# Optimization experiments

Hardware: AMD Instinct MI355X
Metric: run time of the kernel (lower is better)

## Reference

```python
import jax, jax.numpy as jnp
import numpy as np

ALPHA, BETA, LAMB = 1.0, 1.0, 1e-4
K, TAU, DELTA = 16, 0.1, 1e-4
N, D, B, NQ = 100000, 256, 256, 4096


def setup_inputs() -> dict:
    key = jax.random.key(0)
    k1, k2, k3, k4, k5, k6 = jax.random.split(key, 6)
    X = jax.random.normal(k1, (N, D), dtype=jnp.float32)
    W = jax.random.normal(k2, (D, D), dtype=jnp.float32) / np.sqrt(D)
    q_batch = jax.random.normal(k3, (B, D), dtype=jnp.float32)
    pre_weights = jax.random.uniform(k4, (NQ, K), dtype=jnp.float32)
    pre_weights = pre_weights / pre_weights.sum(axis=1, keepdims=True)
    q_indices = jax.random.randint(k5, (B,), 0, NQ)
    pre_indices = jax.random.randint(k6, (NQ, K), 0, N)
    return {"X": X, "W": W, "q_batch": q_batch, "pre_weights": pre_weights,
            "q_indices": q_indices, "pre_indices": pre_indices}


def _matrix_sqrt(A):
    # differentiable symmetric matrix sqrt via eigendecomposition
    w, v = jnp.linalg.eigh(A)
    w = jnp.sqrt(jnp.clip(w, 0.0))
    return (v * w) @ v.T


def _loss_dist(T, mu_X, cov_X, cov_X_sqrt):
    mu = jnp.mean(T, axis=0)
    Tc = T - mu
    cov = Tc.T @ Tc / T.shape[0] + DELTA * jnp.eye(T.shape[1], dtype=T.dtype)
    loss_mean = jnp.sum((mu - mu_X) ** 2)
    cov_sqrt = _matrix_sqrt(cov)
    sqrt_term = _matrix_sqrt(cov_sqrt @ cov_X @ cov_sqrt)
    loss_cov = jnp.trace(cov_X + cov - 2.0 * sqrt_term)
    return jnp.clip(loss_mean + loss_cov, 0.0)


def _kl_per_sample(pre_idx, pre_w, post_idx, post_w):
    # union via first-occurrence mask over concatenated candidates [2K]
    cand = jnp.concatenate([pre_idx, post_idx])
    eq = cand[:, None] == cand[None, :]
    first = ~jnp.tril(eq, k=-1).any(axis=1)
    p = (cand[:, None] == pre_idx[None, :]).astype(pre_w.dtype) @ pre_w
    q = (cand[:, None] == post_idx[None, :]).astype(post_w.dtype) @ post_w
    p = jnp.where(first, jnp.clip(p, 1e-8), 0.0)
    p = p / p.sum()
    q = jnp.where(first, jnp.clip(q, 1e-8), 0.0)
    q = q / q.sum()
    logp = jnp.log(jnp.where(first, p, 1.0))
    logq = jnp.log(jnp.where(first, q, 1.0))
    return jnp.sum(jnp.where(first, p * (logp - logq), 0.0))


def _forward(X, W, q_batch, pre_weights, q_indices, pre_indices):
    # precomputed database stats
    mu_X = jnp.mean(X, axis=0)
    Xc = X - mu_X
    cov_X = Xc.T @ Xc / X.shape[0] + DELTA * jnp.eye(X.shape[1], dtype=X.dtype)
    cov_X_sqrt = _matrix_sqrt(cov_X)

    T = q_batch @ W  # model(q_batch): [B, D]

    loss_dist = _loss_dist(T, mu_X, cov_X, cov_X_sqrt)

    # brute-force exact KNN (faiss flat L2) on detached T
    Td = jax.lax.stop_gradient(T)
    d2 = (jnp.sum(Td * Td, axis=1, keepdims=True)
          - 2.0 * (Td @ X.T) + jnp.sum(X * X, axis=1))  # [B, N]
    _, post_idx = jax.lax.top_k(-d2, K)  # [B, K]

    X_nb = X[post_idx]  # [B, K, D]
    l2 = jnp.sum((T[:, None, :] - X_nb) ** 2, axis=-1)  # [B, K], with grad
    post_w = jax.nn.softmax(-l2 / TAU, axis=1)

    pre_idx_b = pre_indices[q_indices]   # [B, K]
    pre_w_b = pre_weights[q_indices]     # [B, K]
    kls = jax.vmap(_kl_per_sample)(pre_idx_b, pre_w_b, post_idx, post_w)
    loss_knn = jnp.mean(kls)

    loss_reg = 0.5 * jnp.sum(W ** 2)

    total = ALPHA * loss_dist + BETA * loss_knn + LAMB * loss_reg
    return total, loss_dist, loss_knn


def reference(X, W, q_batch, pre_weights, q_indices, pre_indices):
    return _forward(X, W, q_batch, pre_weights, q_indices, pre_indices)
```

## Files before the change

### kernel.cpp

```cpp
#include <hip/hip_runtime.h>

#define NPTS   100000
#define DIMD   256
#define BQ     256
#define PCHUNK 128
#define NPCH   782
#define NCAND  (NPCH*16)
#define NS_ITERS 26
#define KSPLIT  32
#define KSLICE  3136
#define KS2    576
#define NZ2    175

#define SC_LM   0
#define SC_TRCX 1
#define SC_TRCT 2
#define SC_FROB 3
#define SC_KNN  4
#define SC_REG  5
#define SC_LD   6

#define BIGF 3.4e38f

typedef __attribute__((ext_vector_type(4))) float f32x4;
typedef __attribute__((ext_vector_type(8))) unsigned short u16x8;
typedef __attribute__((ext_vector_type(8))) __bf16 bf16x8;

static __device__ __forceinline__ unsigned short f2bf(float f) {
    unsigned u = __float_as_uint(f);
    unsigned r = (u + 0x7fffu + ((u >> 16) & 1u)) >> 16;
    return (unsigned short)r;
}
static __device__ __forceinline__ float bf2f(unsigned short h) {
    return __uint_as_float(((unsigned)h) << 16);
}
static __device__ __forceinline__ unsigned pack_hi(float a, float b) {
    return (__float_as_uint(a) >> 16) | (__float_as_uint(b) & 0xffff0000u);
}
static __device__ __forceinline__ float trunc_bf(float a) {
    return __uint_as_float(__float_as_uint(a) & 0xffff0000u);
}
static __device__ __forceinline__ unsigned short top16(float v) {
    return (unsigned short)(__float_as_uint(v) >> 16);
}
static __device__ __forceinline__ f32x4 mfma16(u16x8 a, u16x8 b, f32x4 c) {
    return __builtin_amdgcn_mfma_f32_16x16x32_bf16(
        __builtin_bit_cast(bf16x8, a), __builtin_bit_cast(bf16x8, b), c, 0, 0, 0);
}

static __device__ __forceinline__ unsigned enc_f32(float f) {
    unsigned u = __float_as_uint(f);
    return u ^ (unsigned)(((int)u >> 31) | 0x80000000);
}
static __device__ __forceinline__ float dec_f32(unsigned e) {
    unsigned u = e ^ ((e & 0x80000000u) ? 0x80000000u : 0xFFFFFFFFu);
    return __uint_as_float(u);
}
static __device__ __forceinline__ unsigned umin32(unsigned a, unsigned b) { return a < b ? a : b; }
static __device__ __forceinline__ void ceu(unsigned& a, unsigned& b) {
    unsigned lo = a < b ? a : b;
    unsigned hi = a < b ? b : a;
    a = lo; b = hi;
}
static __device__ __forceinline__ void sort16(unsigned* r) {
#pragma unroll
    for (int k = 2; k <= 16; k <<= 1)
#pragma unroll
        for (int j = k >> 1; j > 0; j >>= 1)
#pragma unroll
            for (int i = 0; i < 16; ++i) {
                int l = i ^ j;
                if (l > i) {
                    if ((i & k) == 0) ceu(r[i], r[l]);
                    else              ceu(r[l], r[i]);
                }
            }
}
static __device__ __forceinline__ void clean16(unsigned* r) {
#pragma unroll
    for (int j = 8; j > 0; j >>= 1)
#pragma unroll
        for (int i = 0; i < 16; ++i) {
            int l = i ^ j;
            if (l > i) ceu(r[i], r[l]);
        }
}
static __device__ __forceinline__ int lessp(float ka, int ia, float kb, int ib) {
    return (ka < kb) || (ka == kb && ia < ib);
}
static __device__ __forceinline__ void ceup(float& ka, int& ia, float& kb, int& ib) {
    bool sw = lessp(kb, ib, ka, ia);
    float t0 = sw ? kb : ka, t1 = sw ? ka : kb;
    int   u0 = sw ? ib : ia, u1 = sw ? ia : ib;
    ka = t0; kb = t1; ia = u0; ib = u1;
}
static __device__ __forceinline__ void cleanp16(float* k, int* i) {
#pragma unroll
    for (int j = 8; j > 0; j >>= 1)
#pragma unroll
        for (int x = 0; x < 16; ++x) {
            int l = x ^ j;
            if (l > x) ceup(k[x], i[x], k[l], i[l]);
        }
}

__global__ __launch_bounds__(256) void zero_kernel(float* ws) {
    int idx = blockIdx.x * 256 + threadIdx.x;
    if (idx < 66560) ws[idx] = 0.0f;
}

__global__ __launch_bounds__(256) void statsx_kernel(const float* __restrict__ X,
                                                     float* __restrict__ xsq,
                                                     float* __restrict__ mu_sum,
                                                     unsigned short* __restrict__ XHs,
                                                     unsigned short* __restrict__ XLs) {
    __shared__ float colred[4][256];
    const int t = threadIdx.x;
    const int w = t >> 6, lane = t & 63;
    const int half = lane >> 5;
    const int g = lane & 31;
    const int rbase = blockIdx.x * 128;
    float cs[8] = {0.f, 0.f, 0.f, 0.f, 0.f, 0.f, 0.f, 0.f};
#pragma unroll 2
    for (int m = 0; m < 16; ++m) {
        const int r = rbase + m * 8 + w * 2 + half;
        if (r < NPTS) {
            float4 v0 = *(const float4*)&X[r * DIMD + g * 8];
            float4 v1 = *(const float4*)&X[r * DIMD + g * 8 + 4];
            cs[0] += v0.x; cs[1] += v0.y; cs[2] += v0.z; cs[3] += v0.w;
            cs[4] += v1.x; cs[5] += v1.y; cs[6] += v1.z; cs[7] += v1.w;
            float ss = v0.x * v0.x + v0.y * v0.y + v0.z * v0.z + v0.w * v0.w
                     + v1.x * v1.x + v1.y * v1.y + v1.z * v1.z + v1.w * v1.w;
#pragma unroll
            for (int off = 16; off; off >>= 1) ss += __shfl_down(ss, off, 32);
            if (g == 0) xsq[r] = ss;
            if (XHs) {
                uint4 hv = make_uint4(pack_hi(v0.x, v0.y), pack_hi(v0.z, v0.w),
                                      pack_hi(v1.x, v1.y), pack_hi(v1.z, v1.w));
                uint4 lv = make_uint4(
                    pack_hi(v0.x - trunc_bf(v0.x), v0.y - trunc_bf(v0.y)),
                    pack_hi(v0.z - trunc_bf(v0.z), v0.w - trunc_bf(v0.w)),
                    pack_hi(v1.x - trunc_bf(v1.x), v1.y - trunc_bf(v1.y)),
                    pack_hi(v1.z - trunc_bf(v1.z), v1.w - trunc_bf(v1.w)));
                *(uint4*)(XHs + (size_t)r * 256 + g * 8) = hv;
                *(uint4*)(XLs + (size_t)r * 256 + g * 8) = lv;
            }
        } else if (XHs) {
            uint4 z4 = make_uint4(0u, 0u, 0u, 0u);
            *(uint4*)(XHs + (size_t)r * 256 + g * 8) = z4;
            *(uint4*)(XLs + (size_t)r * 256 + g * 8) = z4;
        }
    }
#pragma unroll
    for (int j = 0; j < 8; ++j) cs[j] += __shfl_down(cs[j], 32);
    if (half == 0) {
#pragma unroll
        for (int j = 0; j < 8; ++j) colred[w][g * 8 + j] = cs[j];
    }
    __syncthreads();
    float s = colred[0][t] + colred[1][t] + colred[2][t] + colred[3][t];
    atomicAdd(&mu_sum[t], s);
}

__global__ __launch_bounds__(256) void xtk_kernel(const unsigned short* __restrict__ XHs,
                                                  const unsigned short* __restrict__ XLs,
                                                  unsigned short* __restrict__ XTH,
                                                  unsigned short* __restrict__ XTL) {
    __shared__ unsigned short LH[32][268];
    __shared__ unsigned short LL[32][268];
    const int t = threadIdx.x;
#pragma unroll 1
    for (int st = 0; st < 8; ++st) {
        const int r0 = blockIdx.x * 256 + st * 32;
        const int row = t >> 3;
        const int r = r0 + row;
#pragma unroll
        for (int gg = 0; gg < 4; ++gg) {
            int glog = (t & 7) + gg * 8;
            u16x8 h = *(const u16x8*)(XHs + (size_t)r * 256 + glog * 8);
            u16x8 l = *(const u16x8*)(XLs + (size_t)r * 256 + glog * 8);
            *(u16x8*)&LH[row][glog * 8] = h;
            *(u16x8*)&LL[row][glog * 8] = l;
        }
        __syncthreads();
        {
            unsigned pk[16];
#pragma unroll
            for (int m = 0; m < 16; ++m)
                pk[m] = (unsigned)LH[2 * m][t] | ((unsigned)LH[2 * m + 1][t] << 16);
            uint4* oh = (uint4*)(XTH + (size_t)t * 100352 + r0);
#pragma unroll
            for (int q = 0; q < 4; ++q)
                oh[q] = make_uint4(pk[4 * q], pk[4 * q + 1], pk[4 * q + 2], pk[4 * q + 3]);
#pragma unroll
            for (int m = 0; m < 16; ++m)
                pk[m] = (unsigned)LL[2 * m][t] | ((unsigned)LL[2 * m + 1][t] << 16);
            uint4* ol = (uint4*)(XTL + (size_t)t * 100352 + r0);
#pragma unroll
            for (int q = 0; q < 4; ++q)
                ol[q] = make_uint4(pk[4 * q], pk[4 * q + 1], pk[4 * q + 2], pk[4 * q + 3]);
        }
        __syncthreads();
    }
}

__global__ __launch_bounds__(256) void covx2_kernel(const unsigned short* __restrict__ XTH,
                                                    const unsigned short* __restrict__ XTL,
                                                    float* __restrict__ acc_out) {
    const int quad = blockIdx.x;
    const int qi = quad >> 1, qj = quad & 1;
    const int t = threadIdx.x, w = t >> 6, lane = t & 63;
    const int l15 = lane & 15, l4 = lane >> 4;
    const int k0 = blockIdx.y * KS2;
    const int kend = (k0 + KS2 < 100352) ? (k0 + KS2) : 100352;
    f32x4 acc[2][8];
#pragma unroll
    for (int f = 0; f < 2; ++f)
#pragma unroll
        for (int cf = 0; cf < 8; ++cf) { f32x4 z = {0.f, 0.f, 0.f, 0.f}; acc[f][cf] = z; }
    const size_t rowA0 = (size_t)(qi * 128 + w * 32 + l15) * 100352;
    const size_t rowA1 = (size_t)(qi * 128 + w * 32 + 16 + l15) * 100352;
#pragma unroll 1
    for (int k = k0; k < kend; k += 32) {
        const int ko = k + l4 * 8;
        u16x8 ah0 = *(const u16x8*)(XTH + rowA0 + ko);
        u16x8 al0 = *(const u16x8*)(XTL + rowA0 + ko);
        u16x8 ah1 = *(const u16x8*)(XTH + rowA1 + ko);
        u16x8 al1 = *(const u16x8*)(XTL + rowA1 + ko);
#pragma unroll
        for (int cf = 0; cf < 8; ++cf) {
            const size_t rb = (size_t)(qj * 128 + cf * 16 + l15) * 100352 + ko;
            u16x8 bh = *(const u16x8*)(XTH + rb);
            u16x8 bl = *(const u16x8*)(XTL + rb);
            acc[0][cf] = mfma16(ah0, bh, acc[0][cf]);
            acc[0][cf] = mfma16(ah0, bl, acc[0][cf]);
            acc[0][cf] = mfma16(al0, bh, acc[0][cf]);
            acc[1][cf] = mfma16(ah1, bh, acc[1][cf]);
            acc[1][cf] = mfma16(ah1, bl, acc[1][cf]);
            acc[1][cf] = mfma16(al1, bh, acc[1][cf]);
        }
    }
#pragma unroll
    for (int f = 0; f < 2; ++f)
#pragma unroll
        for (int cf = 0; cf < 8; ++cf)
#pragma unroll
            for (int i = 0; i < 4; ++i) {
                const int r = qi * 128 + w * 32 + f * 16 + l4 * 4 + i;
                const int c = qj * 128 + cf * 16 + l15;
                atomicAdd(&acc_out[r * DIMD + c], acc[f][cf][i]);
            }
}

__global__ __launch_bounds__(256) void covx_kernel(const float* __restrict__ X,
                                                   float* __restrict__ acc_out) {
    __shared__ float Ais[16][64];
    __shared__ float Ajs[16][64];
    int t = threadIdx.x;
    int i0 = blockIdx.x * 64, j0 = blockIdx.y * 64;
    int ks = blockIdx.z * KSLICE;
    int lr = t >> 4, lc = (t & 15) * 4;
    int tx = t & 15, ty = t >> 4;
    float acc[4][4] = {};
    for (int kb = 0; kb < KSLICE; kb += 16) {
        int k = ks + kb + lr;
        if (k < NPTS) {
            float4 vi = *(const float4*)&X[k * DIMD + i0 + lc];
            float4 vj = *(const float4*)&X[k * DIMD + j0 + lc];
            *(float4*)&Ais[lr][lc] = vi;
            *(float4*)&Ajs[lr][lc] = vj;
        } else {
            float4 z = {0.f, 0.f, 0.f, 0.f};
            *(float4*)&Ais[lr][lc] = z;
            *(float4*)&Ajs[lr][lc] = z;
        }
        __syncthreads();
#pragma unroll
        for (int kk = 0; kk < 16; ++kk) {
            float4 a = *(float4*)&Ais[kk][tx * 4];
            float4 b = *(float4*)&Ajs[kk][ty * 4];
            float av[4] = {a.x, a.y, a.z, a.w};
            float bv[4] = {b.x, b.y, b.z, b.w};
#pragma unroll
            for (int m = 0; m < 4; ++m)
#pragma unroll
                for (int n = 0; n < 4; ++n) acc[m][n] += av[m] * bv[n];
        }
        __syncthreads();
    }
#pragma unroll
    for (int m = 0; m < 4; ++m)
#pragma unroll
        for (int n = 0; n < 4; ++n)
            atomicAdd(&acc_out[(i0 + 4 * tx + m) * DIMD + j0 + 4 * ty + n], acc[m][n]);
}

__global__ __launch_bounds__(256) void covxfin2_kernel(const float* __restrict__ acc,
                                                       const float* __restrict__ mu_sum,
                                                       float* __restrict__ covXf,
                                                       float* __restrict__ scal) {
    int idx = blockIdx.x * 256 + threadIdx.x;
    int i = idx >> 8, j = idx & 255;
    const float invN = 1.0f / (float)NPTS;
    float v = acc[idx] * invN - (mu_sum[i] * invN) * (mu_sum[j] * invN) + ((i == j) ? 1e-4f : 0.0f);
    covXf[idx] = v;
    if (i == j) atomicAdd(&scal[SC_TRCX], v);
}

__global__ __launch_bounds__(256) void mm32_kernel(const float* A, const float* B, float* C, const float* D,
                                                   const float* A2, const float* B2, float* C2, const float* D2,
                                                   int mode, const float* mu, float* scal) {
    __shared__ float As[32][32];
    __shared__ float Bs[32][32];
    __shared__ float red[256];
    int t = threadIdx.x;
    int tx = t & 15, ty = t >> 4;
    int i0 = blockIdx.x * 32, j0 = blockIdx.y * 32;
    int lr = t >> 3, lc = (t & 7) * 4;
    float acc[2][2] = {};
    for (int kb = 0; kb < 256; kb += 32) {
        if (mode == 2) {
            float4 v = *(const float4*)&A[(kb + lr) * DIMD + i0 + lc];
            *(float4*)&As[lr][lc] = v;
        } else {
            float4 v = *(const float4*)&A[(i0 + lr) * DIMD + kb + lc];
            As[lc + 0][lr] = v.x; As[lc + 1][lr] = v.y; As[lc + 2][lr] = v.z; As[lc + 3][lr] = v.w;
        }
        {
            float4 v = *(const float4*)&B[(kb + lr) * DIMD + j0 + lc];
            *(float4*)&Bs[lr][lc] = v;
        }
        __syncthreads();
#pragma unroll
        for (int kk = 0; kk < 32; ++kk) {
            float a0 = As[kk][2 * tx], a1 = As[kk][2 * tx + 1];
            float b0 = Bs[kk][2 * ty], b1 = Bs[kk][2 * ty + 1];
            acc[0][0] += a0 * b0; acc[0][1] += a0 * b1;
            acc[1][0] += a1 * b0; acc[1][1] += a1 * b1;
        }
        __syncthreads();
    }
    float fr = 0.f;
#pragma unroll
    for (int ii = 0; ii < 2; ++ii)
#pragma unroll
        for (int jj = 0; jj < 2; ++jj) {
            int i = i0 + 2 * tx + ii, j = j0 + 2 * ty + jj;
            float v = acc[ii][jj];
            if (mode == 2) {
                v = v * (1.0f / 256.0f) - mu[i] * mu[j] + ((i == j) ? 1e-4f : 0.0f);
                if (i == j) atomicAdd(&scal[SC_TRCT], v);
            }
            C[i * DIMD + j] = v;
            if (mode == 1) fr += v * v;
        }
    if (mode == 0 && C2 != nullptr) {
        unsigned short* TH = (unsigned short*)C2;
        unsigned short* TL = (unsigned short*)const_cast<float*>(D2);
#pragma unroll
        for (int ii = 0; ii < 2; ++ii) {
            int i = i0 + 2 * tx + ii;
            int jc = j0 + 2 * ty;
            float x0 = acc[ii][0], x1 = acc[ii][1];
            *(unsigned*)&TH[i * DIMD + jc] = pack_hi(x0, x1);
            *(unsigned*)&TL[i * DIMD + jc] = pack_hi(x0 - trunc_bf(x0), x1 - trunc_bf(x1));
        }
    }
    if (mode == 1) {
        red[t] = fr; __syncthreads();
        for (int s2 = 128; s2 > 0; s2 >>= 1) { if (t < s2) red[t] += red[t + s2]; __syncthreads(); }
        if (t == 0) atomicAdd(&scal[SC_FROB], red[0]);
    }
}

__global__ __launch_bounds__(256) void tstats_kernel(const float* __restrict__ Tm,
                                                     const float* __restrict__ mu_sum,
                                                     float* __restrict__ mu_T,
                                                     float* __restrict__ scal) {
    __shared__ float red[256];
    int j = threadIdx.x;
    float s = 0.f;
    for (int b = 0; b < BQ; ++b) s += Tm[b * DIMD + j];
    float mt = s * (1.0f / 256.0f);
    mu_T[j] = mt;
    float d = mt - mu_sum[j] * (1.0f / (float)NPTS);
    red[j] = d * d;
    __syncthreads();
    for (int s2 = 128; s2 > 0; s2 >>= 1) { if (j < s2) red[j] += red[j + s2]; __syncthreads(); }
    if (j == 0) scal[SC_LM] = red[0];
}

__global__ __launch_bounds__(256) void inityz2_kernel(const float* __restrict__ G,
                                                      const float* __restrict__ scal,
                                                      float* __restrict__ Y, float* __restrict__ Z,
                                                      unsigned short* __restrict__ YaH,
                                                      unsigned short* __restrict__ YaL,
                                                      unsigned short* __restrict__ ZaH,
                                                      unsigned short* __restrict__ ZaL) {
    int idx = blockIdx.x * 256 + threadIdx.x;
    float invs = rsqrtf(scal[SC_FROB]);
    float y = G[idx] * invs;
    Y[idx] = y;
    YaH[idx] = top16(y);
    YaL[idx] = top16(y - trunc_bf(y));
    bool dg = ((idx >> 8) == (idx & 255));
    Z[idx] = dg ? 1.0f : 0.0f;
    ZaH[idx] = dg ? (unsigned short)0x3F80 : (unsigned short)0;
    ZaL[idx] = 0;
}

__global__ __launch_bounds__(256) void nsfused_kernel(
        const float* __restrict__ Ycur, const float* __restrict__ Zcur,
        const unsigned short* __restrict__ YH, const unsigned short* __restrict__ YL,
        const unsigned short* __restrict__ ZH, const unsigned short* __restrict__ ZL,
        float* __restrict__ Yn, float* __restrict__ Zn,
        unsigned short* __restrict__ YnH, unsigned short* __restrict__ YnL,
        unsigned short* __restrict__ ZnH, unsigned short* __restrict__ ZnL) {
    __shared__ __align__(16) unsigned short VH[16 * 264];
    __shared__ __align__(16) unsigned short VL[16 * 264];
    __shared__ __align__(16) unsigned short IH[16 * 264];
    __shared__ __align__(16) unsigned short IL[16 * 264];
    const int t = threadIdx.x, w = t >> 6, lane = t & 63;
    const int l15 = lane & 15, l4 = lane >> 4;
    const int j0 = blockIdx.x * 16;
    const unsigned short *M1H, *M1L, *M2H, *M2L, *VsH, *VsL;
    const float* Dm; float* Out; unsigned short *OH, *OL;
    if (blockIdx.y == 0) { M1H = ZH; M1L = ZL; M2H = YH; M2L = YL; VsH = YH; VsL = YL;
                           Dm = Ycur; Out = Yn; OH = YnH; OL = YnL; }
    else                 { M1H = YH; M1L = YL; M2H = ZH; M2L = ZL; VsH = ZH; VsL = ZL;
                           Dm = Zcur; Out = Zn; OH = ZnH; OL = ZnL; }
    {
        const int col = t >> 4, k0 = (t & 15) * 16;
#pragma unroll
        for (int m = 0; m < 8; ++m) {
            const int k = k0 + 2 * m;
            unsigned h0 = VsH[(size_t)k * 256 + j0 + col];
            unsigned h1 = VsH[(size_t)(k + 1) * 256 + j0 + col];
            unsigned l0 = VsL[(size_t)k * 256 + j0 + col];
            unsigned l1 = VsL[(size_t)(k + 1) * 256 + j0 + col];
            *(unsigned*)&VH[col * 264 + k] = h0 | (h1 << 16);
            *(unsigned*)&VL[col * 264 + k] = l0 | (l1 << 16);
        }
    }
    __syncthreads();
    f32x4 acc[4];
#pragma unroll
    for (int f = 0; f < 4; ++f) { f32x4 z = {0.f, 0.f, 0.f, 0.f}; acc[f] = z; }
#pragma unroll
    for (int ks = 0; ks < 8; ++ks) {
        const int bo = l15 * 264 + ks * 32 + l4 * 8;
        u16x8 bh = *(const u16x8*)&VH[bo];
        u16x8 bl = *(const u16x8*)&VL[bo];
#pragma unroll
        for (int f = 0; f < 4; ++f) {
            const size_t ro = (size_t)(w * 64 + f * 16 + l15) * 256 + ks * 32 + l4 * 8;
            u16x8 ah = *(const u16x8*)(M1H + ro);
            u16x8 al = *(const u16x8*)(M1L + ro);
            acc[f] = mfma16(ah, bh, acc[f]);
            acc[f] = mfma16(ah, bl, acc[f]);
            acc[f] = mfma16(al, bh, acc[f]);
        }
    }
#pragma unroll
    for (int f = 0; f < 4; ++f) {
        float v0 = acc[f][0], v1 = acc[f][1], v2 = acc[f][2], v3 = acc[f][3];
        unsigned h01 = pack_hi(v0, v1), h23 = pack_hi(v2, v3);
        unsigned l01 = pack_hi(v0 - trunc_bf(v0), v1 - trunc_bf(v1));
        unsigned l23 = pack_hi(v2 - trunc_bf(v2), v3 - trunc_bf(v3));
        const int ad = l15 * 264 + w * 64 + f * 16 + l4 * 4;
        *(uint2*)&IH[ad] = make_uint2(h01, h23);
        *(uint2*)&IL[ad] = make_uint2(l01, l23);
    }
    __syncthreads();
#pragma unroll
    for (int f = 0; f < 4; ++f) { f32x4 z = {0.f, 0.f, 0.f, 0.f}; acc[f] = z; }
#pragma unroll
    for (int ks = 0; ks < 8; ++ks) {
        const int bo = l15 * 264 + ks * 32 + l4 * 8;
        u16x8 bh = *(const u16x8*)&IH[bo];
        u16x8 bl = *(const u16x8*)&IL[bo];
#pragma unroll
        for (int f = 0; f < 4; ++f) {
            const size_t ro = (size_t)(w * 64 + f * 16 + l15) * 256 + ks * 32 + l4 * 8;
            u16x8 ah = *(const u16x8*)(M2H + ro);
            u16x8 al = *(const u16x8*)(M2L + ro);
            acc[f] = mfma16(ah, bh, acc[f]);
            acc[f] = mfma16(ah, bl, acc[f]);
            acc[f] = mfma16(al, bh, acc[f]);
        }
    }
#pragma unroll
    for (int f = 0; f < 4; ++f)
#pragma unroll
        for (int i = 0; i < 4; ++i) {
            const int r = w * 64 + f * 16 + l4 * 4 + i;
            const int c = j0 + l15;
            float v = 1.5f * Dm[r * 256 + c] - 0.5f * acc[f][i];
            Out[r * 256 + c] = v;
            OH[r * 256 + c] = top16(v);
            OL[r * 256 + c] = top16(v - trunc_bf(v));
        }
}

__global__ __launch_bounds__(256) void findist_kernel(const float* __restrict__ Yfin,
                                                      float* __restrict__ scal) {
    __shared__ float red[256];
    int t = threadIdx.x;
    red[t] = Yfin[t * (DIMD + 1)];
    __syncthreads();
    for (int s2 = 128; s2 > 0; s2 >>= 1) { if (t < s2) red[t] += red[t + s2]; __syncthreads(); }
    if (t == 0) {
        float frobsq = scal[SC_FROB];
        float tr_sqrt = powf(frobsq, 0.25f) * red[0];
        float lc = scal[SC_TRCX] + scal[SC_TRCT] - 2.0f * tr_sqrt;
        scal[SC_LD] = fmaxf(0.0f, scal[SC_LM] + lc);
    }
}

__global__ __launch_bounds__(256) void reg_kernel(const float* __restrict__ W, float* __restrict__ scal) {
    __shared__ float red[256];
    int t = threadIdx.x;
    float s = 0.f;
    int base = blockIdx.x * 1024;
    for (int m = 0; m < 4; ++m) { float w = W[base + m * 256 + t]; s += w * w; }
    red[t] = s;
    __syncthreads();
    for (int s2 = 128; s2 > 0; s2 >>= 1) { if (t < s2) red[t] += red[t + s2]; __syncthreads(); }
    if (t == 0) atomicAdd(&scal[SC_REG], red[0]);
}

__global__ __launch_bounds__(256, 2) void knn3_kernel(const unsigned short* __restrict__ TmH,
                                                      const unsigned short* __restrict__ TmL,
                                                      const unsigned short* __restrict__ XHs,
                                                      const unsigned short* __restrict__ XLs,
                                                      const float* __restrict__ xsq,
                                                      float* __restrict__ ck, int* __restrict__ ci) {
    __shared__ __align__(16) unsigned char sm2[69632];
    unsigned* kt = (unsigned*)(sm2 + 32768);
    const int t = threadIdx.x;
    const int w = t >> 6, lane = t & 63;
    const int l15 = lane & 15, l4 = lane >> 4;
    const int p0 = blockIdx.x * PCHUNK;
    const int swz = (l15 & 7) << 4;

    unsigned sk[16];
#pragma unroll
    for (int s = 0; s < 16; ++s) sk[s] = 0xFFFFFFFFu;

#pragma unroll 1
    for (int pc = 0; pc < 4; ++pc) {
        const int pbase = p0 + pc * 32;
        {
            const uint4* gh = (const uint4*)(XHs + (size_t)pbase * 256);
            const uint4* gl = (const uint4*)(XLs + (size_t)pbase * 256);
#pragma unroll
            for (int r = 0; r < 4; ++r) {
                const int slot = r * 256 + t;
                const int row = slot >> 5, gi = slot & 31;
                const int dst = row * 512 + (((gi ^ (row & 7))) << 4);
                uint4 vh = gh[slot];
                uint4 vl = gl[slot];
                *(uint4*)(sm2 + dst) = vh;
                *(uint4*)(sm2 + 16384 + dst) = vl;
            }
        }
        __syncthreads();
        f32x4 acc[4][2];
#pragma unroll
        for (int f = 0; f < 4; ++f)
#pragma unroll
            for (int pt = 0; pt < 2; ++pt) { f32x4 z = {0.f, 0.f, 0.f, 0.f}; acc[f][pt] = z; }
#pragma unroll
        for (int ks = 0; ks < 8; ++ks) {
            const int g = (((ks * 4 + l4) << 4)) ^ swz;
            const int b0 = l15 * 512 + g;
            const int b1 = (16 + l15) * 512 + g;
            u16x8 bh0 = *(const u16x8*)(sm2 + b0);
            u16x8 bl0 = *(const u16x8*)(sm2 + 16384 + b0);
            u16x8 bh1 = *(const u16x8*)(sm2 + b1);
            u16x8 bl1 = *(const u16x8*)(sm2 + 16384 + b1);
#pragma unroll
            for (int f = 0; f < 4; ++f) {
                const size_t ro = (size_t)(w * 64 + f * 16 + l15) * 256 + ks * 32 + l4 * 8;
                u16x8 ah = *(const u16x8*)(TmH + ro);
                u16x8 al = *(const u16x8*)(TmL + ro);
                acc[f][0] = mfma16(ah, bh0, acc[f][0]);
                acc[f][0] = mfma16(ah, bl0, acc[f][0]);
                acc[f][0] = mfma16(al, bh0, acc[f][0]);
                acc[f][1] = mfma16(ah, bh1, acc[f][1]);
                acc[f][1] = mfma16(ah, bl1, acc[f][1]);
                acc[f][1] = mfma16(al, bh1, acc[f][1]);
            }
        }
#pragma unroll
        for (int pt = 0; pt < 2; ++pt) {
            const int p = pbase + pt * 16 + l15;
            const float xv = xsq[p];
            const bool ok = (p < NPTS);
            const unsigned lidx = (unsigned)(pc * 32 + pt * 16 + l15);
#pragma unroll
            for (int f = 0; f < 4; ++f)
#pragma unroll
                for (int i = 0; i < 4; ++i) {
                    float d2 = ok ? (xv - 2.0f * acc[f][pt][i]) : BIGF;
                    unsigned e = (enc_f32(d2) & 0xFFFFFF80u) | lidx;
                    kt[(w * 64 + f * 16 + l4 * 4 + i) * 36 + pt * 16 + l15] = e;
                }
        }
        __syncthreads();
#pragma unroll
        for (int hb = 0; hb < 2; ++hb) {
            unsigned b[16];
#pragma unroll
            for (int c4 = 0; c4 < 4; ++c4) {
                uint4 v = *(const uint4*)(kt + t * 36 + hb * 16 + c4 * 4);
                b[c4 * 4 + 0] = v.x; b[c4 * 4 + 1] = v.y;
                b[c4 * 4 + 2] = v.z; b[c4 * 4 + 3] = v.w;
            }
            sort16(b);
#pragma unroll
            for (int i = 0; i < 16; ++i) sk[i] = umin32(sk[i], b[15 - i]);
            clean16(sk);
        }
    }
    const int base = t * NCAND + blockIdx.x * 16;
#pragma unroll
    for (int s = 0; s < 16; ++s) {
        ck[base + s] = dec_f32(sk[s] & 0xFFFFFF80u);
        ci[base + s] = p0 + (int)(sk[s] & 127u);
    }
}

static __device__ __forceinline__ void knn_load(const float* __restrict__ X, int p0, int pc, int t,
                                                float4 s0[2], float4 s1[2]) {
#pragma unroll
    for (int rep = 0; rep < 2; ++rep) {
        int g = t + rep * 512;
        int row = g >> 5, c0 = (g & 31) * 8;
        int p = p0 + pc * 32 + row;
        if (p < NPTS) {
            s0[rep] = *(const float4*)&X[p * DIMD + c0];
            s1[rep] = *(const float4*)&X[p * DIMD + c0 + 4];
        } else {
            float4 z = {0.f, 0.f, 0.f, 0.f};
            s0[rep] = z; s1[rep] = z;
        }
    }
}
static __device__ __forceinline__ void knn_write(unsigned short* XH, unsigned short* XL, int t,
                                                 const float4 s0[2], const float4 s1[2]) {
#pragma unroll
    for (int rep = 0; rep < 2; ++rep) {
        int g = t + rep * 512;
        int row = g >> 5, c0 = (g & 31) * 8;
        float f[8] = {s0[rep].x, s0[rep].y, s0[rep].z, s0[rep].w,
                      s1[rep].x, s1[rep].y, s1[rep].z, s1[rep].w};
        u16x8 h, lo;
#pragma unroll
        for (int j = 0; j < 8; ++j) {
            unsigned short hb = f2bf(f[j]);
            h[j] = hb;
            lo[j] = f2bf(f[j] - bf2f(hb));
        }
        *(u16x8*)&XH[row * 264 + c0] = h;
        *(u16x8*)&XL[row * 264 + c0] = lo;
    }
}
__global__ __launch_bounds__(512, 2) void knn_kernel(const float* __restrict__ Tm,
                                                     const float* __restrict__ X,
                                                     const float* __restrict__ xsq,
                                                     float* __restrict__ ck, int* __restrict__ ci) {
    __shared__ __align__(16) unsigned char smem[50688];
    unsigned short* XH = (unsigned short*)smem;
    unsigned short* XL = (unsigned short*)(smem + 16896);
    float* ktf = (float*)smem;
    float* tk  = (float*)(smem + 34304);
    int*   ti  = (int*)  (smem + 42496);
    const int t    = threadIdx.x;
    const int w    = t >> 6;
    const int lane = t & 63;
    const int l15  = lane & 15;
    const int l4   = lane >> 4;
    const int p0   = blockIdx.x * PCHUNK;
    const int q0   = blockIdx.y * 128;
    u16x8 aH[8], aL[8];
    {
        const int q = q0 + w * 16 + l15;
        const float* tq = Tm + q * DIMD + l4 * 8;
#pragma unroll
        for (int ks = 0; ks < 8; ++ks) {
            float4 v0 = *(const float4*)(tq + ks * 32);
            float4 v1 = *(const float4*)(tq + ks * 32 + 4);
            float f[8] = {v0.x, v0.y, v0.z, v0.w, v1.x, v1.y, v1.z, v1.w};
            u16x8 h, lo;
#pragma unroll
            for (int j = 0; j < 8; ++j) {
                unsigned short hb = f2bf(f[j]);
                h[j] = hb;
                lo[j] = f2bf(f[j] - bf2f(hb));
            }
            aH[ks] = h; aL[ks] = lo;
        }
    }
    float worst = BIGF; int wslot = 0;
    float4 s0[2], s1[2];
    knn_load(X, p0, 0, t, s0, s1);
    knn_write(XH, XL, t, s0, s1);
#pragma unroll
    for (int h = 0; h < 2; ++h) {
        f32x4 acc[4];
#pragma unroll
        for (int a2 = 0; a2 < 4; ++a2) { f32x4 z = {0.f, 0.f, 0.f, 0.f}; acc[a2] = z; }
#pragma unroll
        for (int pc2 = 0; pc2 < 2; ++pc2) {
            const int pc = 2 * h + pc2;
            __syncthreads();
            if (pc < 3) knn_load(X, p0, pc + 1, t, s0, s1);
#pragma unroll
            for (int ks = 0; ks < 8; ++ks) {
#pragma unroll
                for (int pt = 0; pt < 2; ++pt) {
                    const int off = (pt * 16 + l15) * 264 + ks * 32 + l4 * 8;
                    u16x8 bh = *(const u16x8*)&XH[off];
                    u16x8 bl = *(const u16x8*)&XL[off];
                    acc[pc2 * 2 + pt] = mfma16(aH[ks], bh, acc[pc2 * 2 + pt]);
                    acc[pc2 * 2 + pt] = mfma16(aH[ks], bl, acc[pc2 * 2 + pt]);
                    acc[pc2 * 2 + pt] = mfma16(aL[ks], bh, acc[pc2 * 2 + pt]);
                }
            }
            __syncthreads();
            if (pc2 == 0 && pc < 3) knn_write(XH, XL, t, s0, s1);
        }
#pragma unroll
        for (int pc2 = 0; pc2 < 2; ++pc2) {
#pragma unroll
            for (int pt = 0; pt < 2; ++pt) {
                const int pl = pc2 * 32 + pt * 16 + l15;
                const int p  = p0 + h * 64 + pl;
                const float xv = (p < NPTS) ? xsq[p] : 0.f;
#pragma unroll
                for (int i = 0; i < 4; ++i) {
                    float key = (p < NPTS) ? (xv - 2.0f * acc[pc2 * 2 + pt][i]) : BIGF;
                    ktf[(w * 16 + l4 * 4 + i) * 67 + pl] = key;
                }
            }
        }
        __syncthreads();
        if (t < 128) {
            if (h == 0) {
#pragma unroll
                for (int s = 0; s < 16; ++s) { tk[s * 128 + t] = BIGF; ti[s * 128 + t] = 0x7fffffff; }
            }
            for (int c = 0; c < 64; ++c) {
                float key = ktf[t * 67 + c];
                if (key < worst) {
                    tk[wslot * 128 + t] = key; ti[wslot * 128 + t] = p0 + h * 64 + c;
                    worst = tk[t]; wslot = 0;
#pragma unroll
                    for (int s = 1; s < 16; ++s) {
                        float v = tk[s * 128 + t];
                        if (v > worst) { worst = v; wslot = s; }
                    }
                }
            }
        }
        __syncthreads();
        if (h == 0) knn_write(XH, XL, t, s0, s1);
    }
    if (t < 128) {
        int base = (q0 + t) * NCAND + blockIdx.x * 16;
        for (int s = 0; s < 16; ++s) { ck[base + s] = tk[s * 128 + t]; ci[base + s] = ti[s * 128 + t]; }
    }
}

__global__ __launch_bounds__(256) void merge2_kernel(const float* __restrict__ ck,
                                                     const int* __restrict__ ci,
                                                     int* __restrict__ post_idx) {
    __shared__ float km[16 * 256];
    __shared__ int   im[16 * 256];
    const int q = blockIdx.x, t = threadIdx.x;
    float sk[16]; int si[16];
#pragma unroll
    for (int s = 0; s < 16; ++s) { sk[s] = BIGF; si[s] = 0x7fffffff; }
#pragma unroll 1
    for (int run = t; run < NPCH; run += 256) {
        const float* rk = ck + (size_t)q * NCAND + run * 16;
        const int*   ri = ci + (size_t)q * NCAND + run * 16;
#pragma unroll 1
        for (int s = 0; s < 16; ++s) {
            float k = rk[s]; int id = ri[s];
            if (!lessp(k, id, sk[15], si[15])) break;
#pragma unroll
            for (int j = 15; j > 0; --j) {
                bool a = lessp(k, id, sk[j - 1], si[j - 1]);
                bool b = lessp(k, id, sk[j], si[j]);
                float nk = a ? sk[j - 1] : (b ? k : sk[j]);
                int   ni = a ? si[j - 1] : (b ? id : si[j]);
                sk[j] = nk; si[j] = ni;
            }
            bool c = lessp(k, id, sk[0], si[0]);
            float nk0 = c ? k : sk[0]; int ni0 = c ? id : si[0];
            sk[0] = nk0; si[0] = ni0;
        }
    }
#pragma unroll
    for (int s = 0; s < 16; ++s) { km[s * 256 + t] = sk[s]; im[s * 256 + t] = si[s]; }
    __syncthreads();
    for (int off = 128; off > 0; off >>= 1) {
        if (t < off) {
            float bk[16]; int bi[16];
#pragma unroll
            for (int s = 0; s < 16; ++s) { bk[s] = km[s * 256 + t + off]; bi[s] = im[s * 256 + t + off]; }
#pragma unroll
            for (int s = 0; s < 16; ++s) {
                float ak = sk[s];  int ai = si[s];
                float ok = bk[15 - s]; int oi = bi[15 - s];
                bool a = lessp(ak, ai, ok, oi);
                sk[s] = a ? ak : ok; si[s] = a ? ai : oi;
            }
            cleanp16(sk, si);
#pragma unroll
            for (int s = 0; s < 16; ++s) { km[s * 256 + t] = sk[s]; im[s * 256 + t] = si[s]; }
        }
        __syncthreads();
    }
    if (t == 0) {
#pragma unroll
        for (int r = 0; r < 16; ++r) post_idx[q * 16 + r] = si[r];
    }
}

__global__ __launch_bounds__(256) void merge_kernel(const float* __restrict__ ck,
                                                    const int* __restrict__ ci,
                                                    int* __restrict__ post_idx) {
    __shared__ float tk[16][256];
    __shared__ int   ti[16][256];
    __shared__ float rk[256];
    __shared__ int   ri[256];
    __shared__ int   rt2[256];
    __shared__ int   rs2[256];
    int q = blockIdx.x, t = threadIdx.x;
    for (int s = 0; s < 16; ++s) { tk[s][t] = BIGF; ti[s][t] = 0x7fffffff; }
    float worst = BIGF; int wslot = 0;
    for (int e = t; e < NCAND; e += 256) {
        float key = ck[q * NCAND + e];
        if (key < worst) {
            tk[wslot][t] = key; ti[wslot][t] = ci[q * NCAND + e];
            worst = tk[0][t]; wslot = 0;
            for (int s = 1; s < 16; ++s)
                if (tk[s][t] > worst) { worst = tk[s][t]; wslot = s; }
        }
    }
    __syncthreads();
    for (int r = 0; r < 16; ++r) {
        float bk = tk[0][t]; int bi = ti[0][t], bs = 0;
        for (int s = 1; s < 16; ++s) {
            float k2 = tk[s][t]; int i2 = ti[s][t];
            if (k2 < bk || (k2 == bk && i2 < bi)) { bk = k2; bi = i2; bs = s; }
        }
        rk[t] = bk; ri[t] = bi; rt2[t] = t; rs2[t] = bs;
        __syncthreads();
        for (int s2 = 128; s2 > 0; s2 >>= 1) {
            if (t < s2) {
                float ko = rk[t + s2]; int io = ri[t + s2];
                if (ko < rk[t] || (ko == rk[t] && io < ri[t])) {
                    rk[t] = ko; ri[t] = io; rt2[t] = rt2[t + s2]; rs2[t] = rs2[t + s2];
                }
            }
            __syncthreads();
        }
        if (t == rt2[0]) { tk[rs2[0]][t] = BIGF; ti[rs2[0]][t] = 0x7fffffff; }
        if (t == 0) post_idx[q * 16 + r] = ri[0];
        __syncthreads();
    }
}

__global__ __launch_bounds__(256) void l2sm_kernel(const float* __restrict__ Tm,
                                                   const float* __restrict__ X,
                                                   const int* __restrict__ post_idx,
                                                   float* __restrict__ post_w) {
    __shared__ float l2s[16];
    int b = blockIdx.x, t = threadIdx.x;
    int k = t >> 4, j = t & 15;
    int idx = post_idx[b * 16 + k];
    float s = 0.f;
    for (int i = 0; i < 16; ++i) {
        int d = j + 16 * i;
        float df = Tm[b * DIMD + d] - X[idx * DIMD + d];
        s += df * df;
    }
    for (int off = 8; off; off >>= 1) s += __shfl_down(s, off, 16);
    if (j == 0) l2s[k] = s;
    __syncthreads();
    if (t < 16) {
        float x = -l2s[t] * 10.0f;
        float m = x;
        for (int mm = 8; mm; mm >>= 1) m = fmaxf(m, __shfl_xor(m, mm, 16));
        float e = expf(x - m);
        float ssum = e;
        for (int mm = 8; mm; mm >>= 1) ssum += __shfl_xor(ssum, mm, 16);
        post_w[b * 16 + t] = e / ssum;
    }
}

__global__ __launch_bounds__(256) void kl_kernel(const int* __restrict__ q_indices,
                                                 const int* __restrict__ pre_indices,
                                                 const float* __restrict__ pre_weights,
                                                 const int* __restrict__ post_idx,
                                                 const float* __restrict__ post_w,
                                                 float* __restrict__ scal) {
    int b = threadIdx.x;
    int qi = q_indices[b];
    int pid[16]; float pw[16]; int sid[16]; float sw[16];
    for (int k = 0; k < 16; ++k) {
        pid[k] = pre_indices[qi * 16 + k];
        pw[k]  = pre_weights[qi * 16 + k];
        sid[k] = post_idx[b * 16 + k];
        sw[k]  = post_w[b * 16 + k];
    }
    float psum = 0.f, qsum = 0.f, kl = 0.f;
    for (int pass = 0; pass < 2; ++pass) {
        for (int i = 0; i < 32; ++i) {
            int c = (i < 16) ? pid[i] : sid[i - 16];
            bool first = true;
            for (int jj = 0; jj < i; ++jj) {
                int cj = (jj < 16) ? pid[jj] : sid[jj - 16];
                if (cj == c) { first = false; break; }
            }
            if (!first) continue;
            float p = 0.f, q = 0.f;
            for (int k2 = 0; k2 < 16; ++k2) {
                if (pid[k2] == c) p += pw[k2];
                if (sid[k2] == c) q += sw[k2];
            }
            p = fmaxf(p, 1e-8f); q = fmaxf(q, 1e-8f);
            if (pass == 0) { psum += p; qsum += q; }
            else {
                float pn = p / psum, qn = q / qsum;
                kl += pn * (logf(pn) - logf(qn));
            }
        }
    }
    atomicAdd(&scal[SC_KNN], kl * (1.0f / 256.0f));
}

__global__ void assemble_kernel(const float* __restrict__ scal, float* __restrict__ out) {
    if (threadIdx.x == 0) {
        float ld = scal[SC_LD], lk = scal[SC_KNN], reg = scal[SC_REG];
        out[0] = ld + lk + 1e-4f * 0.5f * reg;
        out[1] = ld;
        out[2] = lk;
    }
}

extern "C" void kernel_launch(void* const* d_in, const int* in_sizes, int n_in,
                              void* d_out, int out_size, void* d_ws, size_t ws_size,
                              hipStream_t stream) {
    (void)in_sizes; (void)n_in; (void)out_size;
    const float* X           = (const float*)d_in[0];
    const float* W           = (const float*)d_in[1];
    const float* q_batch     = (const float*)d_in[2];
    const float* pre_weights = (const float*)d_in[3];
    const int*   q_indices   = (const int*)d_in[4];
    const int*   pre_indices = (const int*)d_in[5];
    float* out = (float*)d_out;
    float* ws  = (float*)d_ws;

    float* mu_sum = ws + 0;
    float* scal   = ws + 256;
    float* mu_T   = ws + 512;
    float* covX   = ws + 1024;
    float* Tm     = ws + 66560;
    float* cov    = ws + 132096;
    float* G      = ws + 197632;
    float* Ya     = ws + 263168;
    float* Za     = ws + 328704;
    float* Yb     = ws + 394240;
    float* Zb     = ws + 459776;
    float* covXf  = ws + 525312;
    float* xsq    = ws + 590848;
    float* post_w = ws + 691200;
    int*   post_idx = (int*)(ws + 695296);
    float* ck     = ws + 699392;
    int*   ci     = (int*)(ws + 3902464);
    unsigned short* YaH = (unsigned short*)(ws + 699392);
    unsigned short* YaL = (unsigned short*)(ws + 732160);
    unsigned short* ZaH = (unsigned short*)(ws + 764928);
    unsigned short* ZaL = (unsigned short*)(ws + 797696);
    unsigned short* YbH = (unsigned short*)(ws + 830464);
    unsigned short* YbL = (unsigned short*)(ws + 863232);
    unsigned short* ZbH = (unsigned short*)(ws + 896000);
    unsigned short* ZbL = (unsigned short*)(ws + 928768);
    unsigned short* XHs = (unsigned short*)(ws + 7105536);
    unsigned short* XLs = (unsigned short*)(ws + 19950592);
    unsigned short* TmH = (unsigned short*)(ws + 32795648);
    unsigned short* TmL = (unsigned short*)(ws + 32828416);
    unsigned short* XTH = (unsigned short*)(ws + 32845824);
    unsigned short* XTL = (unsigned short*)(ws + 45690880);
    const bool haveIMG = (ws_size >= (size_t)131444736);
    const bool haveXT  = (ws_size >= (size_t)234143744);

    zero_kernel<<<260, 256, 0, stream>>>(ws);
    reg_kernel<<<64, 256, 0, stream>>>(W, scal);
    statsx_kernel<<<784, 256, 0, stream>>>(X, xsq, mu_sum,
                                           haveIMG ? XHs : nullptr, haveIMG ? XLs : nullptr);
    if (haveXT) {
        xtk_kernel<<<392, 256, 0, stream>>>(XHs, XLs, XTH, XTL);
        covx2_kernel<<<dim3(4, NZ2), 256, 0, stream>>>(XTH, XTL, covX);
    } else {
        covx_kernel<<<dim3(4, 4, KSPLIT), 256, 0, stream>>>(X, covX);
    }
    covxfin2_kernel<<<256, 256, 0, stream>>>(covX, mu_sum, covXf, scal);
    mm32_kernel<<<dim3(8, 8, 1), 256, 0, stream>>>(q_batch, W, Tm, nullptr,
                                                   nullptr, nullptr,
                                                   haveIMG ? (float*)TmH : nullptr,
                                                   haveIMG ? (float*)TmL : nullptr, 0, nullptr, scal);
    tstats_kernel<<<1, 256, 0, stream>>>(Tm, mu_sum, mu_T, scal);
    mm32_kernel<<<dim3(8, 8, 1), 256, 0, stream>>>(Tm, Tm, cov, nullptr,
                                                   nullptr, nullptr, nullptr, nullptr, 2, mu_T, scal);
    mm32_kernel<<<dim3(8, 8, 1), 256, 0, stream>>>(cov, covXf, G, nullptr,
                                                   nullptr, nullptr, nullptr, nullptr, 1, nullptr, scal);
    if (haveIMG) {
        knn3_kernel<<<NPCH, 256, 0, stream>>>(TmH, TmL, XHs, XLs, xsq, ck, ci);
        merge2_kernel<<<256, 256, 0, stream>>>(ck, ci, post_idx);
    } else {
        knn_kernel<<<dim3(NPCH, 2, 1), 512, 0, stream>>>(Tm, X, xsq, ck, ci);
        merge_kernel<<<256, 256, 0, stream>>>(ck, ci, post_idx);
    }
    l2sm_kernel<<<256, 256, 0, stream>>>(Tm, X, post_idx, post_w);
    kl_kernel<<<1, 256, 0, stream>>>(q_indices, pre_indices, pre_weights, post_idx, post_w, scal);
    inityz2_kernel<<<256, 256, 0, stream>>>(G, scal, Ya, Za, YaH, YaL, ZaH, ZaL);
    {
        float *Yc = Ya, *Zc = Za, *Yn = Yb, *Zn = Zb;
        unsigned short *cYH = YaH, *cYL = YaL, *cZH = ZaH, *cZL = ZaL;
        unsigned short *nYH = YbH, *nYL = YbL, *nZH = ZbH, *nZL = ZbL;
        for (int it = 0; it < NS_ITERS; ++it) {
            nsfused_kernel<<<dim3(16, 2), 256, 0, stream>>>(Yc, Zc, cYH, cYL, cZH, cZL,
                                                            Yn, Zn, nYH, nYL, nZH, nZL);
            float* tf;
            tf = Yc; Yc = Yn; Yn = tf;
            tf = Zc; Zc = Zn; Zn = tf;
            unsigned short* tu;
            tu = cYH; cYH = nYH; nYH = tu;
            tu = cYL; cYL = nYL; nYL = tu;
            tu = cZH; cZH = nZH; nZH = tu;
            tu = cZL; cZL = nZL; nZL = tu;
        }
        findist_kernel<<<1, 256, 0, stream>>>(Yc, scal);
    }
    assemble_kernel<<<1, 64, 0, stream>>>(scal, out);
}
```

Before: 1.379 ms.

## Persistent Newton-Schulz kernel with grid barrier; symmetric covariance blocks

The 26 separate Newton-Schulz launches are folded into one persistent 32-block kernel. It synchronises between iterations with an atomic grid barrier, which removes per-launch overhead. Because cov_X is symmetric, the covariance GEMM now computes only 3 of its 4 quadrant blocks, and the finalize step mirrors the missing lower-left block. The K-slice is also made smaller to launch more blocks, with unroll 2. The risks are a barrier that needs all 32 blocks co-resident and a zero-initialised counter in scal, and that the final Y lands in Ya only because NS_ITERS is even.

```diff
diff --git a/kernel.cpp b/kernel.cpp
--- a/kernel.cpp
+++ b/kernel.cpp
@@ -9,8 +9,8 @@
 #define NS_ITERS 26
 #define KSPLIT  32
 #define KSLICE  3136
-#define KS2    576
-#define NZ2    175
+#define KS2    384
+#define NZ2    262
 
 #define SC_LM   0
 #define SC_TRCX 1
@@ -207,8 +207,9 @@
 __global__ __launch_bounds__(256) void covx2_kernel(const unsigned short* __restrict__ XTH,
                                                     const unsigned short* __restrict__ XTL,
                                                     float* __restrict__ acc_out) {
-    const int quad = blockIdx.x;
-    const int qi = quad >> 1, qj = quad & 1;
+    const int bq = blockIdx.x;
+    const int qi = bq >> 1;
+    const int qj = (bq + 1) >> 1;
     const int t = threadIdx.x, w = t >> 6, lane = t & 63;
     const int l15 = lane & 15, l4 = lane >> 4;
     const int k0 = blockIdx.y * KS2;
@@ -220,7 +221,7 @@
         for (int cf = 0; cf < 8; ++cf) { f32x4 z = {0.f, 0.f, 0.f, 0.f}; acc[f][cf] = z; }
     const size_t rowA0 = (size_t)(qi * 128 + w * 32 + l15) * 100352;
     const size_t rowA1 = (size_t)(qi * 128 + w * 32 + 16 + l15) * 100352;
-#pragma unroll 1
+#pragma unroll 2
     for (int k = k0; k < kend; k += 32) {
         const int ko = k + l4 * 8;
         u16x8 ah0 = *(const u16x8*)(XTH + rowA0 + ko);
@@ -298,11 +299,12 @@
 __global__ __launch_bounds__(256) void covxfin2_kernel(const float* __restrict__ acc,
                                                        const float* __restrict__ mu_sum,
                                                        float* __restrict__ covXf,
-                                                       float* __restrict__ scal) {
+                                                       float* __restrict__ scal, int sym) {
     int idx = blockIdx.x * 256 + threadIdx.x;
     int i = idx >> 8, j = idx & 255;
+    int src = (sym && i >= 128 && j < 128) ? (j * DIMD + i) : idx;
     const float invN = 1.0f / (float)NPTS;
-    float v = acc[idx] * invN - (mu_sum[i] * invN) * (mu_sum[j] * invN) + ((i == j) ? 1e-4f : 0.0f);
+    float v = acc[src] * invN - (mu_sum[i] * invN) * (mu_sum[j] * invN) + ((i == j) ? 1e-4f : 0.0f);
     covXf[idx] = v;
     if (i == j) atomicAdd(&scal[SC_TRCX], v);
 }
@@ -409,97 +411,131 @@
     ZaL[idx] = 0;
 }
 
-__global__ __launch_bounds__(256) void nsfused_kernel(
-        const float* __restrict__ Ycur, const float* __restrict__ Zcur,
-        const unsigned short* __restrict__ YH, const unsigned short* __restrict__ YL,
-        const unsigned short* __restrict__ ZH, const unsigned short* __restrict__ ZL,
-        float* __restrict__ Yn, float* __restrict__ Zn,
-        unsigned short* __restrict__ YnH, unsigned short* __restrict__ YnL,
-        unsigned short* __restrict__ ZnH, unsigned short* __restrict__ ZnL) {
+__global__ __launch_bounds__(256) void nsall_kernel(
+        float* __restrict__ Ya, float* __restrict__ Za,
+        float* __restrict__ Yb, float* __restrict__ Zb,
+        unsigned short* __restrict__ YaH, unsigned short* __restrict__ YaL,
+        unsigned short* __restrict__ ZaH, unsigned short* __restrict__ ZaL,
+        unsigned short* __restrict__ YbH, unsigned short* __restrict__ YbL,
+        unsigned short* __restrict__ ZbH, unsigned short* __restrict__ ZbL,
+        unsigned* __restrict__ bar) {
     __shared__ __align__(16) unsigned short VH[16 * 264];
     __shared__ __align__(16) unsigned short VL[16 * 264];
     __shared__ __align__(16) unsigned short IH[16 * 264];
     __shared__ __align__(16) unsigned short IL[16 * 264];
     const int t = threadIdx.x, w = t >> 6, lane = t & 63;
     const int l15 = lane & 15, l4 = lane >> 4;
-    const int j0 = blockIdx.x * 16;
-    const unsigned short *M1H, *M1L, *M2H, *M2L, *VsH, *VsL;
-    const float* Dm; float* Out; unsigned short *OH, *OL;
-    if (blockIdx.y == 0) { M1H = ZH; M1L = ZL; M2H = YH; M2L = YL; VsH = YH; VsL = YL;
-                           Dm = Ycur; Out = Yn; OH = YnH; OL = YnL; }
-    else                 { M1H = YH; M1L = YL; M2H = ZH; M2L = ZL; VsH = ZH; VsL = ZL;
-                           Dm = Zcur; Out = Zn; OH = ZnH; OL = ZnL; }
-    {
-        const int col = t >> 4, k0 = (t & 15) * 16;
-#pragma unroll
-        for (int m = 0; m < 8; ++m) {
-            const int k = k0 + 2 * m;
-            unsigned h0 = VsH[(size_t)k * 256 + j0 + col];
-            unsigned h1 = VsH[(size_t)(k + 1) * 256 + j0 + col];
-            unsigned l0 = VsL[(size_t)k * 256 + j0 + col];
-            unsigned l1 = VsL[(size_t)(k + 1) * 256 + j0 + col];
-            *(unsigned*)&VH[col * 264 + k] = h0 | (h1 << 16);
-            *(unsigned*)&VL[col * 264 + k] = l0 | (l1 << 16);
-        }
-    }
-    __syncthreads();
-    f32x4 acc[4];
-#pragma unroll
-    for (int f = 0; f < 4; ++f) { f32x4 z = {0.f, 0.f, 0.f, 0.f}; acc[f] = z; }
-#pragma unroll
-    for (int ks = 0; ks < 8; ++ks) {
-        const int bo = l15 * 264 + ks * 32 + l4 * 8;
-        u16x8 bh = *(const u16x8*)&VH[bo];
-        u16x8 bl = *(const u16x8*)&VL[bo];
+    const int bid = blockIdx.x;
+    const int path = bid >> 4;
+    const int j0 = (bid & 15) * 16;
+    const int nb = (int)gridDim.x;
+
+#pragma unroll 1
+    for (int it = 0; it < NS_ITERS; ++it) {
+        const int par = it & 1;
+        const float* Ycur = par ? Yb : Ya;
+        const float* Zcur = par ? Zb : Za;
+        float* Yn = par ? Ya : Yb;
+        float* Zn = par ? Za : Zb;
+        const unsigned short* YH = par ? YbH : YaH;
+        const unsigned short* YL = par ? YbL : YaL;
+        const unsigned short* ZH = par ? ZbH : ZaH;
+        const unsigned short* ZL = par ? ZbL : ZaL;
+        unsigned short* YnH = par ? YaH : YbH;
+        unsigned short* YnL = par ? YaL : YbL;
+        unsigned short* ZnH = par ? ZaH : ZbH;
+        unsigned short* ZnL = par ? ZaL : ZbL;
+        const unsigned short *M1H, *M1L, *M2H, *M2L, *VsH, *VsL;
+        const float* Dm; float* Out; unsigned short *OH, *OL;
+        if (path == 0) { M1H = ZH; M1L = ZL; M2H = YH; M2L = YL; VsH = YH; VsL = YL;
+                         Dm = Ycur; Out = Yn; OH = YnH; OL = YnL; }
+        else           { M1H = YH; M1L = YL; M2H = ZH; M2L = ZL; VsH = ZH; VsL = ZL;
+                         Dm = Zcur; Out = Zn; OH = ZnH; OL = ZnL; }
+        {
+            const int col = t >> 4, k0 = (t & 15) * 16;
+#pragma unroll
+            for (int m = 0; m < 8; ++m) {
+                const int k = k0 + 2 * m;
+                unsigned h0 = VsH[(size_t)k * 256 + j0 + col];
+                unsigned h1 = VsH[(size_t)(k + 1) * 256 + j0 + col];
+                unsigned l0 = VsL[(size_t)k * 256 + j0 + col];
+                unsigned l1 = VsL[(size_t)(k + 1) * 256 + j0 + col];
+                *(unsigned*)&VH[col * 264 + k] = h0 | (h1 << 16);
+                *(unsigned*)&VL[col * 264 + k] = l0 | (l1 << 16);
+            }
+        }
+        __syncthreads();
+        f32x4 acc[4];
+#pragma unroll
+        for (int f = 0; f < 4; ++f) { f32x4 z = {0.f, 0.f, 0.f, 0.f}; acc[f] = z; }
+#pragma unroll
+        for (int ks = 0; ks < 8; ++ks) {
+            const int bo = l15 * 264 + ks * 32 + l4 * 8;
+            u16x8 bh = *(const u16x8*)&VH[bo];
+            u16x8 bl = *(const u16x8*)&VL[bo];
+#pragma unroll
+            for (int f = 0; f < 4; ++f) {
+                const size_t ro = (size_t)(w * 64 + f * 16 + l15) * 256 + ks * 32 + l4 * 8;
+                u16x8 ah = *(const u16x8*)(M1H + ro);
+                u16x8 al = *(const u16x8*)(M1L + ro);
+                acc[f] = mfma16(ah, bh, acc[f]);
+                acc[f] = mfma16(ah, bl, acc[f]);
+                acc[f] = mfma16(al, bh, acc[f]);
+            }
+        }
 #pragma unroll
         for (int f = 0; f < 4; ++f) {
-            const size_t ro = (size_t)(w * 64 + f * 16 + l15) * 256 + ks * 32 + l4 * 8;
-            u16x8 ah = *(const u16x8*)(M1H + ro);
-            u16x8 al = *(const u16x8*)(M1L + ro);
-            acc[f] = mfma16(ah, bh, acc[f]);
-            acc[f] = mfma16(ah, bl, acc[f]);
-            acc[f] = mfma16(al, bh, acc[f]);
-        }
-    }
-#pragma unroll
-    for (int f = 0; f < 4; ++f) {
-        float v0 = acc[f][0], v1 = acc[f][1], v2 = acc[f][2], v3 = acc[f][3];
-        unsigned h01 = pack_hi(v0, v1), h23 = pack_hi(v2, v3);
-        unsigned l01 = pack_hi(v0 - trunc_bf(v0), v1 - trunc_bf(v1));
-        unsigned l23 = pack_hi(v2 - trunc_bf(v2), v3 - trunc_bf(v3));
-        const int ad = l15 * 264 + w * 64 + f * 16 + l4 * 4;
-        *(uint2*)&IH[ad] = make_uint2(h01, h23);
-        *(uint2*)&IL[ad] = make_uint2(l01, l23);
-    }
-    __syncthreads();
-#pragma unroll
-    for (int f = 0; f < 4; ++f) { f32x4 z = {0.f, 0.f, 0.f, 0.f}; acc[f] = z; }
-#pragma unroll
-    for (int ks = 0; ks < 8; ++ks) {
-        const int bo = l15 * 264 + ks * 32 + l4 * 8;
-        u16x8 bh = *(const u16x8*)&IH[bo];
-        u16x8 bl = *(const u16x8*)&IL[bo];
-#pragma unroll
-        for (int f = 0; f < 4; ++f) {
-            const size_t ro = (size_t)(w * 64 + f * 16 + l15) * 256 + ks * 32 + l4 * 8;
-            u16x8 ah = *(const u16x8*)(M2H + ro);
-            u16x8 al = *(const u16x8*)(M2L + ro);
-            acc[f] = mfma16(ah, bh, acc[f]);
-            acc[f] = mfma16(ah, bl, acc[f]);
-            acc[f] = mfma16(al, bh, acc[f]);
-        }
-    }
-#pragma unroll
-    for (int f = 0; f < 4; ++f)
-#pragma unroll
-        for (int i = 0; i < 4; ++i) {
-            const int r = w * 64 + f * 16 + l4 * 4 + i;
-            const int c = j0 + l15;
-            float v = 1.5f * Dm[r * 256 + c] - 0.5f * acc[f][i];
-            Out[r * 256 + c] = v;
-            OH[r * 256 + c] = top16(v);
-            OL[r * 256 + c] = top16(v - trunc_bf(v));
-        }
+            float v0 = acc[f][0], v1 = acc[f][1], v2 = acc[f][2], v3 = acc[f][3];
+            unsigned h01 = pack_hi(v0, v1), h23 = pack_hi(v2, v3);
+            unsigned l01 = pack_hi(v0 - trunc_bf(v0), v1 - trunc_bf(v1));
+            unsigned l23 = pack_hi(v2 - trunc_bf(v2), v3 - trunc_bf(v3));
+            const int ad = l15 * 264 + w * 64 + f * 16 + l4 * 4;
+            *(uint2*)&IH[ad] = make_uint2(h01, h23);
+            *(uint2*)&IL[ad] = make_uint2(l01, l23);
+        }
+        __syncthreads();
+#pragma unroll
+        for (int f = 0; f < 4; ++f) { f32x4 z = {0.f, 0.f, 0.f, 0.f}; acc[f] = z; }
+#pragma unroll
+        for (int ks = 0; ks < 8; ++ks) {
+            const int bo = l15 * 264 + ks * 32 + l4 * 8;
+            u16x8 bh = *(const u16x8*)&IH[bo];
+            u16x8 bl = *(const u16x8*)&IL[bo];
+#pragma unroll
+            for (int f = 0; f < 4; ++f) {
+                const size_t ro = (size_t)(w * 64 + f * 16 + l15) * 256 + ks * 32 + l4 * 8;
+                u16x8 ah = *(const u16x8*)(M2H + ro);
+                u16x8 al = *(const u16x8*)(M2L + ro);
+                acc[f] = mfma16(ah, bh, acc[f]);
+                acc[f] = mfma16(ah, bl, acc[f]);
+                acc[f] = mfma16(al, bh, acc[f]);
+            }
+        }
+#pragma unroll
+        for (int f = 0; f < 4; ++f)
+#pragma unroll
+            for (int i = 0; i < 4; ++i) {
+                const int r = w * 64 + f * 16 + l4 * 4 + i;
+                const int c = j0 + l15;
+                float v = 1.5f * Dm[r * 256 + c] - 0.5f * acc[f][i];
+                Out[r * 256 + c] = v;
+                OH[r * 256 + c] = top16(v);
+                OL[r * 256 + c] = top16(v - trunc_bf(v));
+            }
+        __threadfence();
+        __syncthreads();
+        if (t == 0) {
+            unsigned g = atomicAdd(&bar[1], 0u);
+            if (atomicAdd(&bar[0], 1u) == (unsigned)(nb - 1)) {
+                atomicExch(&bar[0], 0u);
+                atomicAdd(&bar[1], 1u);
+            } else {
+                while (atomicAdd(&bar[1], 0u) == g) { __builtin_amdgcn_s_sleep(2); }
+            }
+        }
+        __syncthreads();
+        __threadfence();
+    }
 }
 
 __global__ __launch_bounds__(256) void findist_kernel(const float* __restrict__ Yfin,
@@ -997,6 +1033,7 @@
     unsigned short* TmL = (unsigned short*)(ws + 32828416);
     unsigned short* XTH = (unsigned short*)(ws + 32845824);
     unsigned short* XTL = (unsigned short*)(ws + 45690880);
+    unsigned* nsbar = (unsigned*)(scal + 32);
     const bool haveIMG = (ws_size >= (size_t)131444736);
     const bool haveXT  = (ws_size >= (size_t)234143744);
 
@@ -1006,11 +1043,11 @@
                                            haveIMG ? XHs : nullptr, haveIMG ? XLs : nullptr);
     if (haveXT) {
         xtk_kernel<<<392, 256, 0, stream>>>(XHs, XLs, XTH, XTL);
-        covx2_kernel<<<dim3(4, NZ2), 256, 0, stream>>>(XTH, XTL, covX);
+        covx2_kernel<<<dim3(3, NZ2), 256, 0, stream>>>(XTH, XTL, covX);
     } else {
         covx_kernel<<<dim3(4, 4, KSPLIT), 256, 0, stream>>>(X, covX);
     }
-    covxfin2_kernel<<<256, 256, 0, stream>>>(covX, mu_sum, covXf, scal);
+    covxfin2_kernel<<<256, 256, 0, stream>>>(covX, mu_sum, covXf, scal, haveXT ? 1 : 0);
     mm32_kernel<<<dim3(8, 8, 1), 256, 0, stream>>>(q_batch, W, Tm, nullptr,
                                                    nullptr, nullptr,
                                                    haveIMG ? (float*)TmH : nullptr,
@@ -1030,23 +1067,9 @@
     l2sm_kernel<<<256, 256, 0, stream>>>(Tm, X, post_idx, post_w);
     kl_kernel<<<1, 256, 0, stream>>>(q_indices, pre_indices, pre_weights, post_idx, post_w, scal);
     inityz2_kernel<<<256, 256, 0, stream>>>(G, scal, Ya, Za, YaH, YaL, ZaH, ZaL);
-    {
-        float *Yc = Ya, *Zc = Za, *Yn = Yb, *Zn = Zb;
-        unsigned short *cYH = YaH, *cYL = YaL, *cZH = ZaH, *cZL = ZaL;
-        unsigned short *nYH = YbH, *nYL = YbL, *nZH = ZbH, *nZL = ZbL;
-        for (int it = 0; it < NS_ITERS; ++it) {
-            nsfused_kernel<<<dim3(16, 2), 256, 0, stream>>>(Yc, Zc, cYH, cYL, cZH, cZL,
-                                                            Yn, Zn, nYH, nYL, nZH, nZL);
-            float* tf;
-            tf = Yc; Yc = Yn; Yn = tf;
-            tf = Zc; Zc = Zn; Zn = tf;
-            unsigned short* tu;
-            tu = cYH; cYH = nYH; nYH = tu;
-            tu = cYL; cYL = nYL; nYL = tu;
-            tu = cZH; cZH = nZH; nZH = tu;
-            tu = cZL; cZL = nZL; nZL = tu;
-        }
-        findist_kernel<<<1, 256, 0, stream>>>(Yc, scal);
-    }
+    nsall_kernel<<<32, 256, 0, stream>>>(Ya, Za, Yb, Zb,
+                                         YaH, YaL, ZaH, ZaL,
+                                         YbH, YbL, ZbH, ZbL, nsbar);
+    findist_kernel<<<1, 256, 0, stream>>>(Ya, scal);
     assemble_kernel<<<1, 64, 0, stream>>>(scal, out);
 }
```

After: 1.578 ms. 1.14x slower.
